# Kernel optimization log

Measured on AMD Instinct MI355X. Metric: run time of the kernel, lower is better.

The kernel has to match this reference:

```python
import jax, jax.numpy as jnp
import numpy as np
import math

SIZE = 2048
N_CLASSES = 16
STEPS = 100
DT = 0.03
GAMMA = 0.125
BETA = 1.0
EIG = 1.0
EPSILON = 0.1


def _make_P(size=SIZE, n_classes=N_CLASSES):
    # Default attractor construction: block indicator columns.
    attr = np.zeros((size, n_classes), dtype=np.float32)
    block = size // n_classes
    for c in range(n_classes):
        attr[c * block:(c + 1) * block, c] = 1.0
    norm_attr = attr / (np.linalg.norm(attr, axis=0, keepdims=True) + 1e-8) ** 2
    return jnp.asarray(norm_attr @ attr.T)  # [size, size] projection onto attractor subspace


def setup_inputs() -> dict:
    key = jax.random.key(0)
    kx, ka, kg, kn = jax.random.split(key, 4)
    x = jax.random.normal(kx, (512, SIZE), dtype=jnp.float32)
    # kaiming_uniform_(a=sqrt(5)) => U(-1/sqrt(fan_in), 1/sqrt(fan_in))
    bound = 1.0 / math.sqrt(SIZE)
    A = jax.random.uniform(ka, (SIZE, SIZE), minval=-bound, maxval=bound, dtype=jnp.float32)
    G = jax.random.uniform(kg, (SIZE, SIZE), minval=-bound, maxval=bound, dtype=jnp.float32)
    noise = jax.random.normal(kn, (STEPS, 512, SIZE), dtype=jnp.float32)
    return {"x": x, "A": A, "G": G, "noise": noise}


def reference(x, A, G, noise):
    P = _make_P()
    antiP = jnp.eye(SIZE, dtype=x.dtype) - P
    B = (A @ antiP + EIG * P).T  # [size, size]
    GT = G.T
    sqrt_dt = math.sqrt(DT)

    def nl(x):
        x2 = x * x
        return x2 / (GAMMA + x2)

    def step(x, n):
        x_dot = -x + BETA * (nl(x) @ B)
        x_new = x + DT * x_dot + sqrt_dt * EPSILON * (n @ GT)
        return x_new, None

    x_final, _ = jax.lax.scan(step, x, noise)
    return x_final
```

## Files before the change

### kernel.cpp

```cpp
#include <hip/hip_runtime.h>
#include <cstdint>


typedef unsigned short ushort_t;
typedef __bf16 bf16x8 __attribute__((ext_vector_type(8)));
typedef float f32x4 __attribute__((ext_vector_type(4)));
typedef unsigned short u16x4 __attribute__((ext_vector_type(4)));
typedef unsigned short u16x8 __attribute__((ext_vector_type(8)));

#define SZ 2048
#define BATCH 512
#define NSTEPS 100

static constexpr float DT = 0.03f;
static constexpr float GAM = 0.125f;
static constexpr float PVAL = (float)(1.0 / (128.0 + 2.2627416997969522e-07));
static constexpr float CNOISE = 0.017320508075688773f;

__device__ __forceinline__ unsigned short f2bf(float f) {
    unsigned int u = __builtin_bit_cast(unsigned int, f);
    return (unsigned short)((u + 0x7fffu + ((u >> 16) & 1u)) >> 16);
}
__device__ __forceinline__ float bf2f(unsigned short h) {
    unsigned int u = ((unsigned int)h) << 16;
    return __builtin_bit_cast(float, u);
}
__device__ __forceinline__ void async16(const void* g, void* l) {
    __builtin_amdgcn_global_load_lds(
        (__attribute__((address_space(1))) void*)(uintptr_t)g,
        (__attribute__((address_space(3))) void*)(uint32_t)(uintptr_t)l,
        16, 0, 0);
}

__global__ __launch_bounds__(256) void conv_kernel(const float* __restrict__ n,
                                                   ushort_t* __restrict__ nb) {
    const size_t i = ((size_t)blockIdx.x * 256 + threadIdx.x) * 4;
    f32x4 v = *(const f32x4*)(n + i);
    u16x4 o;
#pragma unroll
    for (int e = 0; e < 4; ++e) o[e] = f2bf(v[e]);
    *(u16x4*)(nb + i) = o;
}

__global__ __launch_bounds__(256) void prep_kernel(const float* __restrict__ A,
                                                   const float* __restrict__ G,
                                                   ushort_t* __restrict__ BTs,
                                                   ushort_t* __restrict__ Gs) {
    const int n = blockIdx.x;
    const int t = threadIdx.x;
    __shared__ float s16[16];
    const float* arow = A + (size_t)n * SZ;
    f32x4 a0 = *(const f32x4*)(arow + t * 8);
    f32x4 a1 = *(const f32x4*)(arow + t * 8 + 4);
    float ps = a0[0] + a0[1] + a0[2] + a0[3] + a1[0] + a1[1] + a1[2] + a1[3];
#pragma unroll
    for (int m = 1; m < 16; m <<= 1) ps += __shfl_xor(ps, m, 64);
    if ((t & 15) == 0) s16[t >> 4] = ps * PVAL;
    __syncthreads();
    const int seg = t >> 4;
    const float s = s16[seg];
    const float diag = (seg == (n >> 7)) ? PVAL : 0.0f;
    float av[8] = {a0[0], a0[1], a0[2], a0[3], a1[0], a1[1], a1[2], a1[3]};
    u16x8 ov;
#pragma unroll
    for (int i = 0; i < 8; ++i) ov[i] = f2bf(DT * (av[i] - s + diag));
    *(u16x8*)&BTs[(size_t)n * SZ + t * 8] = ov;

    const float* grow = G + (size_t)n * SZ;
    f32x4 g0 = *(const f32x4*)(grow + t * 8);
    f32x4 g1 = *(const f32x4*)(grow + t * 8 + 4);
    float gv[8] = {g0[0], g0[1], g0[2], g0[3], g1[0], g1[1], g1[2], g1[3]};
    u16x8 og;
#pragma unroll
    for (int i = 0; i < 8; ++i) og[i] = f2bf(CNOISE * gv[i]);
    *(u16x8*)&Gs[(size_t)n * SZ + t * 8] = og;
}

__global__ __launch_bounds__(256) void init_kernel(const float* __restrict__ x,
                                                   float* __restrict__ xbuf,
                                                   ushort_t* __restrict__ Y0) {
    const size_t i = ((size_t)blockIdx.x * 256 + threadIdx.x) * 4;
    f32x4 xv = *(const f32x4*)(x + i);
    *(f32x4*)(xbuf + i) = xv;
    u16x4 yv;
#pragma unroll
    for (int e = 0; e < 4; ++e) {
        float x2 = xv[e] * xv[e];
        yv[e] = f2bf(x2 / (GAM + x2));
    }
    *(u16x4*)(Y0 + i) = yv;
}

__global__ __launch_bounds__(256) void zgemm_kernel(const ushort_t* __restrict__ Nb,
                                                    const ushort_t* __restrict__ Gs,
                                                    ushort_t* __restrict__ Z) {
    __shared__ ushort_t sm[16384];
    const int tid = threadIdx.x;
    const int w = tid >> 6, l = tid & 63;
    const int m0 = blockIdx.y << 7, n0 = blockIdx.x << 7;
    const char* Ag = (const char*)Nb + (size_t)m0 * 4096;
    const char* Bg = (const char*)Gs + (size_t)n0 * 4096;
    const int goff = (tid >> 3) * 4096 + (((tid & 7) ^ ((tid >> 3) & 7)) << 4);
    const int loff = tid * 16;
    const int lr = l & 15, q8 = l >> 4;
    const int wm = (w & 1) << 6, wn = (w >> 1) << 6;
    const int swz = lr & 7;
    f32x4 acc[4][4] = {};

    char* sA = (char*)sm;
    char* sB = sA + 16384;
    for (int kk = 0; kk < 32; ++kk) {
        __syncthreads();
        const char* Ac = Ag + kk * 128;
        const char* Bc = Bg + kk * 128;
#pragma unroll
        for (int i = 0; i < 4; ++i) {
            async16(Ac + i * 131072 + goff, sA + i * 4096 + loff);
            async16(Bc + i * 131072 + goff, sB + i * 4096 + loff);
        }
        asm volatile("s_waitcnt vmcnt(0)" ::: "memory");
        __syncthreads();
#pragma unroll
        for (int half = 0; half < 2; ++half) {
            const int qpos = ((((half << 2) | q8) ^ swz) << 4);
            bf16x8 af[4], bfv[4];
#pragma unroll
            for (int f = 0; f < 4; ++f) {
                af[f] = *(const bf16x8*)(sA + (wm + f * 16 + lr) * 128 + qpos);
                bfv[f] = *(const bf16x8*)(sB + (wn + f * 16 + lr) * 128 + qpos);
            }
#pragma unroll
            for (int fr = 0; fr < 4; ++fr)
#pragma unroll
                for (int fc = 0; fc < 4; ++fc)
                    acc[fr][fc] = __builtin_amdgcn_mfma_f32_16x16x32_bf16(
                        af[fr], bfv[fc], acc[fr][fc], 0, 0, 0);
        }
    }
    ushort_t* zr = Z + (size_t)m0 * SZ + n0;
#pragma unroll
    for (int fr = 0; fr < 4; ++fr)
#pragma unroll
        for (int reg = 0; reg < 4; ++reg) {
            const size_t rb = (size_t)(wm + fr * 16 + q8 * 4 + reg) * SZ;
#pragma unroll
            for (int fc = 0; fc < 4; ++fc)
                zr[rb + wn + fc * 16 + lr] = f2bf(acc[fr][fc][reg]);
        }
}

__global__ __launch_bounds__(512, 2) void step_kernel(
    const ushort_t* __restrict__ Ycur, const ushort_t* __restrict__ BTs,
    const ushort_t* __restrict__ Zt, const float* __restrict__ xin,
    float* __restrict__ xout, ushort_t* __restrict__ Ynext) {
    extern __shared__ ushort_t smem[];
    const int tid = threadIdx.x;
    const int w = tid >> 6, l = tid & 63;
    const int m0 = blockIdx.y << 6, n0 = blockIdx.x << 6;

    const char* Ag = (const char*)Ycur + (size_t)m0 * 4096 + w * 512;
    const char* Bg = (const char*)BTs + (size_t)n0 * 4096 + w * 512;
    char* waveLds = (char*)smem + w * 16384;

    const int goffL = (l >> 2) * 4096 + ((((l & 3) ^ ((l >> 3) & 3))) << 4);
    const int loffL = l * 16;
    const int lr = l & 15, q8 = l >> 4;
    const int swz2 = (lr >> 1) & 3;

    f32x4 acc[4][4] = {};

    auto stage = [&](int ci, int b) {
        const char* Ac = Ag + ci * 64;
        const char* Bc = Bg + ci * 64;
        char* dA = waveLds + b * 8192;
        char* dB = dA + 4096;
#pragma unroll
        for (int i = 0; i < 4; ++i) {
            async16(Ac + i * 65536 + goffL, dA + i * 1024 + loffL);
            async16(Bc + i * 65536 + goffL, dB + i * 1024 + loffL);
        }
    };
    auto compute = [&](int b) {
        const char* TA = waveLds + b * 8192;
        const char* TB = TA + 4096;
        const int qpos = ((q8 ^ swz2) << 4);
        bf16x8 af[4], bfv[4];
#pragma unroll
        for (int f = 0; f < 4; ++f) {
            af[f] = *(const bf16x8*)(TA + (f * 16 + lr) * 64 + qpos);
            bfv[f] = *(const bf16x8*)(TB + (f * 16 + lr) * 64 + qpos);
        }
#pragma unroll
        for (int fr = 0; fr < 4; ++fr)
#pragma unroll
            for (int fc = 0; fc < 4; ++fc)
                acc[fr][fc] = __builtin_amdgcn_mfma_f32_16x16x32_bf16(
                    af[fr], bfv[fc], acc[fr][fc], 0, 0, 0);
    };

    stage(0, 0);
#pragma unroll 2
    for (int ci = 0; ci < 8; ++ci) {
        if (ci < 7) {
            stage(ci + 1, (ci + 1) & 1);
            asm volatile("s_waitcnt vmcnt(8)" ::: "memory");
        } else {
            asm volatile("s_waitcnt vmcnt(0)" ::: "memory");
        }
        compute(ci & 1);
    }

    float* redF = (float*)smem;
#pragma unroll
    for (int p = 0; p < 2; ++p) {
        __syncthreads();
#pragma unroll
        for (int fl = 0; fl < 2; ++fl) {
            const int fr = p * 2 + fl;
            const int rl = fl * 16 + q8 * 4;
#pragma unroll
            for (int fc = 0; fc < 4; ++fc) {
                const int c = fc * 16 + lr;
#pragma unroll
                for (int reg = 0; reg < 4; ++reg)
                    redF[w * 2176 + (rl + reg) * 68 + c] = acc[fr][fc][reg];
            }
        }
        __syncthreads();
        {
            const int r = tid >> 4;
            const int c0 = (tid & 15) << 2;
            const int off = r * 68 + c0;
            f32x4 s = *(const f32x4*)&redF[off];
#pragma unroll
            for (int ww = 1; ww < 8; ++ww)
                s = s + *(const f32x4*)&redF[ww * 2176 + off];
            const size_t gb = (size_t)(m0 + p * 32 + r) * SZ + n0 + c0;
            f32x4 xv = *(const f32x4*)(xin + gb);
            u16x4 zb = *(const u16x4*)(Zt + gb);
            f32x4 xn;
#pragma unroll
            for (int e = 0; e < 4; ++e) xn[e] = xv[e] * (1.0f - DT) + s[e] + bf2f(zb[e]);
            *(f32x4*)(xout + gb) = xn;
            u16x4 yv;
#pragma unroll
            for (int e = 0; e < 4; ++e) {
                float x2 = xn[e] * xn[e];
                yv[e] = f2bf(x2 / (GAM + x2));
            }
            *(u16x4*)(Ynext + gb) = yv;
        }
    }
}

extern "C" void kernel_launch(void* const* d_in, const int* in_sizes, int n_in,
                              void* d_out, int out_size, void* d_ws, size_t ws_size,
                              hipStream_t stream) {
    const float* x = (const float*)d_in[0];
    const float* A = (const float*)d_in[1];
    const float* G = (const float*)d_in[2];
    const float* noise = (const float*)d_in[3];
    float* out = (float*)d_out;
    char* ws = (char*)d_ws;

    float* xbuf = (float*)(ws);
    ushort_t* Y0 = (ushort_t*)(ws + ((size_t)4 << 20));
    ushort_t* Y1 = (ushort_t*)(ws + ((size_t)6 << 20));
    ushort_t* BTs = (ushort_t*)(ws + ((size_t)8 << 20));
    ushort_t* Gsc = (ushort_t*)(ws + ((size_t)16 << 20));
    ushort_t* Nb = (ushort_t*)(ws + ((size_t)24 << 20));
    ushort_t* Z = (ushort_t*)(ws + ((size_t)240 << 20));

    (void)hipFuncSetAttribute((const void*)step_kernel,
                              hipFuncAttributeMaxDynamicSharedMemorySize, 131072);

    conv_kernel<<<dim3(102400), dim3(256), 0, stream>>>(noise, Nb);
    prep_kernel<<<dim3(SZ), dim3(256), 0, stream>>>(A, G, BTs, Gsc);
    init_kernel<<<dim3(1024), dim3(256), 0, stream>>>(x, xbuf, Y0);
    zgemm_kernel<<<dim3(16, 400), dim3(256), 0, stream>>>(Nb, Gsc, Z);

    ushort_t* Yc = Y0;
    ushort_t* Yn = Y1;
    for (int t = 0; t < NSTEPS; ++t) {
        float* xo = (t == NSTEPS - 1) ? out : xbuf;
        step_kernel<<<dim3(32, 8), dim3(512), 131072, stream>>>(
            Yc, BTs, Z + (size_t)t * BATCH * SZ, xbuf, xo, Yn);
        ushort_t* tmp = Yc; Yc = Yn; Yn = tmp;
    }
}
```

Baseline: 2.770 ms.

## Fuse noise GEMM into persistent cooperative step kernel with per-row-group barriers

Replaces the separate noise GEMM and the 100 per-step launches with one cooperative persistent kernel. Each block concatenates the K dimension: four waves multiply Y by B and four multiply the noise slice by G, so the noise term is computed inside the step instead of being stored to and reloaded from a large Z buffer. The x state stays in registers across steps, and blocks synchronise only within their 64-row group through atomic counter barriers. This removes launch overhead and the Z and x global traffic, but doubles the K length of every step and adds spin barriers.

```diff
diff --git a/kernel.cpp b/kernel.cpp
--- a/kernel.cpp
+++ b/kernel.cpp
@@ -20,10 +20,6 @@
 __device__ __forceinline__ unsigned short f2bf(float f) {
     unsigned int u = __builtin_bit_cast(unsigned int, f);
     return (unsigned short)((u + 0x7fffu + ((u >> 16) & 1u)) >> 16);
-}
-__device__ __forceinline__ float bf2f(unsigned short h) {
-    unsigned int u = ((unsigned int)h) << 16;
-    return __builtin_bit_cast(float, u);
 }
 __device__ __forceinline__ void async16(const void* g, void* l) {
     __builtin_amdgcn_global_load_lds(
@@ -77,11 +73,10 @@
 }
 
 __global__ __launch_bounds__(256) void init_kernel(const float* __restrict__ x,
-                                                   float* __restrict__ xbuf,
-                                                   ushort_t* __restrict__ Y0) {
+                                                   ushort_t* __restrict__ Y0,
+                                                   unsigned* __restrict__ bar) {
     const size_t i = ((size_t)blockIdx.x * 256 + threadIdx.x) * 4;
     f32x4 xv = *(const f32x4*)(x + i);
-    *(f32x4*)(xbuf + i) = xv;
     u16x4 yv;
 #pragma unroll
     for (int e = 0; e < 4; ++e) {
@@ -89,45 +84,87 @@
         yv[e] = f2bf(x2 / (GAM + x2));
     }
     *(u16x4*)(Y0 + i) = yv;
-}
-
-__global__ __launch_bounds__(256) void zgemm_kernel(const ushort_t* __restrict__ Nb,
-                                                    const ushort_t* __restrict__ Gs,
-                                                    ushort_t* __restrict__ Z) {
-    __shared__ ushort_t sm[16384];
+    if (blockIdx.x == 0) bar[threadIdx.x] = 0u;
+}
+
+__device__ __forceinline__ void group_barrier(unsigned* cnt, unsigned* gen) {
+    __syncthreads();
+    if (threadIdx.x == 0) {
+        __threadfence();
+        unsigned g = atomicAdd(gen, 0u);
+        if (atomicAdd(cnt, 1u) == 31u) {
+            atomicExch(cnt, 0u);
+            __threadfence();
+            atomicAdd(gen, 1u);
+        } else {
+            while (atomicAdd(gen, 0u) == g) __builtin_amdgcn_s_sleep(8);
+        }
+        __threadfence();
+    }
+    __syncthreads();
+}
+
+__global__ __launch_bounds__(512, 2) void persist_kernel(
+    const float* __restrict__ x0,
+    const ushort_t* __restrict__ BTs, const ushort_t* __restrict__ Gs,
+    const ushort_t* __restrict__ Nb,
+    ushort_t* __restrict__ Y0, ushort_t* __restrict__ Y1,
+    float* __restrict__ xout, unsigned* __restrict__ bar) {
+    extern __shared__ ushort_t smem[];
     const int tid = threadIdx.x;
     const int w = tid >> 6, l = tid & 63;
-    const int m0 = blockIdx.y << 7, n0 = blockIdx.x << 7;
-    const char* Ag = (const char*)Nb + (size_t)m0 * 4096;
-    const char* Bg = (const char*)Gs + (size_t)n0 * 4096;
-    const int goff = (tid >> 3) * 4096 + (((tid & 7) ^ ((tid >> 3) & 7)) << 4);
-    const int loff = tid * 16;
+    const int id = blockIdx.x;
+    const int nIdx = (id & 7) | (((id >> 3) & 3) << 3);
+    const int mIdx = id >> 5;
+    const int m0 = mIdx << 6, n0 = nIdx << 6;
+
+    unsigned* cnt = bar + mIdx * 32;
+    unsigned* gen = cnt + 1;
+
+    const char* Bg = (w < 4)
+        ? ((const char*)BTs + (size_t)n0 * 4096 + w * 1024)
+        : ((const char*)Gs + (size_t)n0 * 4096 + (w - 4) * 1024);
+    char* waveLds = (char*)smem + w * 16384;
+
+    const int goffL = (l >> 2) * 4096 + (((l & 3) ^ ((l >> 3) & 3)) << 4);
+    const int loffL = l * 16;
     const int lr = l & 15, q8 = l >> 4;
-    const int wm = (w & 1) << 6, wn = (w >> 1) << 6;
-    const int swz = lr & 7;
-    f32x4 acc[4][4] = {};
-
-    char* sA = (char*)sm;
-    char* sB = sA + 16384;
-    for (int kk = 0; kk < 32; ++kk) {
-        __syncthreads();
-        const char* Ac = Ag + kk * 128;
-        const char* Bc = Bg + kk * 128;
-#pragma unroll
-        for (int i = 0; i < 4; ++i) {
-            async16(Ac + i * 131072 + goff, sA + i * 4096 + loff);
-            async16(Bc + i * 131072 + goff, sB + i * 4096 + loff);
-        }
-        asm volatile("s_waitcnt vmcnt(0)" ::: "memory");
-        __syncthreads();
-#pragma unroll
-        for (int half = 0; half < 2; ++half) {
-            const int qpos = ((((half << 2) | q8) ^ swz) << 4);
+    const int qpos = (q8 ^ ((lr >> 1) & 3)) << 4;
+
+    const int er = tid >> 4;
+    const int ec0 = (tid & 15) << 2;
+    f32x4 xreg[2];
+    xreg[0] = *(const f32x4*)(x0 + (size_t)(m0 + er) * SZ + n0 + ec0);
+    xreg[1] = *(const f32x4*)(x0 + (size_t)(m0 + 32 + er) * SZ + n0 + ec0);
+
+    for (int t = 0; t < NSTEPS; ++t) {
+        const ushort_t* Yc = (t & 1) ? Y1 : Y0;
+        ushort_t* Yn = (t & 1) ? Y0 : Y1;
+        const char* Ag = (w < 4)
+            ? ((const char*)Yc + (size_t)m0 * 4096 + w * 1024)
+            : ((const char*)Nb + (size_t)t * 2097152 + (size_t)m0 * 4096 + (w - 4) * 1024);
+
+        f32x4 acc[4][4] = {};
+
+        auto stage = [&](int ci, int b) {
+            const char* Ac = Ag + ci * 64;
+            const char* Bc = Bg + ci * 64;
+            char* dA = waveLds + b * 8192;
+            char* dB = dA + 4096;
+#pragma unroll
+            for (int i = 0; i < 4; ++i) {
+                async16(Ac + i * 65536 + goffL, dA + i * 1024 + loffL);
+                async16(Bc + i * 65536 + goffL, dB + i * 1024 + loffL);
+            }
+        };
+        auto compute = [&](int b) {
+            const char* TA = waveLds + b * 8192;
+            const char* TB = TA + 4096;
             bf16x8 af[4], bfv[4];
 #pragma unroll
             for (int f = 0; f < 4; ++f) {
-                af[f] = *(const bf16x8*)(sA + (wm + f * 16 + lr) * 128 + qpos);
-                bfv[f] = *(const bf16x8*)(sB + (wn + f * 16 + lr) * 128 + qpos);
+                af[f] = *(const bf16x8*)(TA + (f * 16 + lr) * 64 + qpos);
+                bfv[f] = *(const bf16x8*)(TB + (f * 16 + lr) * 64 + qpos);
             }
 #pragma unroll
             for (int fr = 0; fr < 4; ++fr)
@@ -135,121 +172,61 @@
                 for (int fc = 0; fc < 4; ++fc)
                     acc[fr][fc] = __builtin_amdgcn_mfma_f32_16x16x32_bf16(
                         af[fr], bfv[fc], acc[fr][fc], 0, 0, 0);
+        };
+
+        stage(0, 0);
+#pragma unroll 2
+        for (int ci = 0; ci < 16; ++ci) {
+            if (ci < 15) {
+                stage(ci + 1, (ci + 1) & 1);
+                asm volatile("s_waitcnt vmcnt(8)" ::: "memory");
+            } else {
+                asm volatile("s_waitcnt vmcnt(0)" ::: "memory");
+            }
+            compute(ci & 1);
         }
-    }
-    ushort_t* zr = Z + (size_t)m0 * SZ + n0;
-#pragma unroll
-    for (int fr = 0; fr < 4; ++fr)
-#pragma unroll
-        for (int reg = 0; reg < 4; ++reg) {
-            const size_t rb = (size_t)(wm + fr * 16 + q8 * 4 + reg) * SZ;
-#pragma unroll
-            for (int fc = 0; fc < 4; ++fc)
-                zr[rb + wn + fc * 16 + lr] = f2bf(acc[fr][fc][reg]);
+
+        float* redF = (float*)smem;
+#pragma unroll
+        for (int p = 0; p < 2; ++p) {
+            __syncthreads();
+#pragma unroll
+            for (int fl = 0; fl < 2; ++fl) {
+                const int fr = p * 2 + fl;
+                const int rl = fl * 16 + q8 * 4;
+#pragma unroll
+                for (int fc = 0; fc < 4; ++fc) {
+                    const int c = fc * 16 + lr;
+#pragma unroll
+                    for (int reg = 0; reg < 4; ++reg)
+                        redF[w * 2176 + (rl + reg) * 68 + c] = acc[p * 2 + fl == fr ? fr : fr][fc][reg];
+                }
+            }
+            __syncthreads();
+            {
+                const int off = er * 68 + ec0;
+                f32x4 s = *(const f32x4*)&redF[off];
+#pragma unroll
+                for (int ww = 1; ww < 8; ++ww)
+                    s = s + *(const f32x4*)&redF[ww * 2176 + off];
+                f32x4 xn = xreg[p] * (1.0f - DT) + s;
+                xreg[p] = xn;
+                const size_t gb = (size_t)(m0 + p * 32 + er) * SZ + n0 + ec0;
+                if (t < NSTEPS - 1) {
+                    u16x4 yv;
+#pragma unroll
+                    for (int e = 0; e < 4; ++e) {
+                        float x2 = xn[e] * xn[e];
+                        yv[e] = f2bf(x2 / (GAM + x2));
+                    }
+                    *(u16x4*)(Yn + gb) = yv;
+                } else {
+                    *(f32x4*)(xout + gb) = xn;
+                }
+            }
         }
-}
-
-__global__ __launch_bounds__(512, 2) void step_kernel(
-    const ushort_t* __restrict__ Ycur, const ushort_t* __restrict__ BTs,
-    const ushort_t* __restrict__ Zt, const float* __restrict__ xin,
-    float* __restrict__ xout, ushort_t* __restrict__ Ynext) {
-    extern __shared__ ushort_t smem[];
-    const int tid = threadIdx.x;
-    const int w = tid >> 6, l = tid & 63;
-    const int m0 = blockIdx.y << 6, n0 = blockIdx.x << 6;
-
-    const char* Ag = (const char*)Ycur + (size_t)m0 * 4096 + w * 512;
-    const char* Bg = (const char*)BTs + (size_t)n0 * 4096 + w * 512;
-    char* waveLds = (char*)smem + w * 16384;
-
-    const int goffL = (l >> 2) * 4096 + ((((l & 3) ^ ((l >> 3) & 3))) << 4);
-    const int loffL = l * 16;
-    const int lr = l & 15, q8 = l >> 4;
-    const int swz2 = (lr >> 1) & 3;
-
-    f32x4 acc[4][4] = {};
-
-    auto stage = [&](int ci, int b) {
-        const char* Ac = Ag + ci * 64;
-        const char* Bc = Bg + ci * 64;
-        char* dA = waveLds + b * 8192;
-        char* dB = dA + 4096;
-#pragma unroll
-        for (int i = 0; i < 4; ++i) {
-            async16(Ac + i * 65536 + goffL, dA + i * 1024 + loffL);
-            async16(Bc + i * 65536 + goffL, dB + i * 1024 + loffL);
-        }
-    };
-    auto compute = [&](int b) {
-        const char* TA = waveLds + b * 8192;
-        const char* TB = TA + 4096;
-        const int qpos = ((q8 ^ swz2) << 4);
-        bf16x8 af[4], bfv[4];
-#pragma unroll
-        for (int f = 0; f < 4; ++f) {
-            af[f] = *(const bf16x8*)(TA + (f * 16 + lr) * 64 + qpos);
-            bfv[f] = *(const bf16x8*)(TB + (f * 16 + lr) * 64 + qpos);
-        }
-#pragma unroll
-        for (int fr = 0; fr < 4; ++fr)
-#pragma unroll
-            for (int fc = 0; fc < 4; ++fc)
-                acc[fr][fc] = __builtin_amdgcn_mfma_f32_16x16x32_bf16(
-                    af[fr], bfv[fc], acc[fr][fc], 0, 0, 0);
-    };
-
-    stage(0, 0);
-#pragma unroll 2
-    for (int ci = 0; ci < 8; ++ci) {
-        if (ci < 7) {
-            stage(ci + 1, (ci + 1) & 1);
-            asm volatile("s_waitcnt vmcnt(8)" ::: "memory");
-        } else {
-            asm volatile("s_waitcnt vmcnt(0)" ::: "memory");
-        }
-        compute(ci & 1);
-    }
-
-    float* redF = (float*)smem;
-#pragma unroll
-    for (int p = 0; p < 2; ++p) {
-        __syncthreads();
-#pragma unroll
-        for (int fl = 0; fl < 2; ++fl) {
-            const int fr = p * 2 + fl;
-            const int rl = fl * 16 + q8 * 4;
-#pragma unroll
-            for (int fc = 0; fc < 4; ++fc) {
-                const int c = fc * 16 + lr;
-#pragma unroll
-                for (int reg = 0; reg < 4; ++reg)
-                    redF[w * 2176 + (rl + reg) * 68 + c] = acc[fr][fc][reg];
-            }
-        }
-        __syncthreads();
-        {
-            const int r = tid >> 4;
-            const int c0 = (tid & 15) << 2;
-            const int off = r * 68 + c0;
-            f32x4 s = *(const f32x4*)&redF[off];
-#pragma unroll
-            for (int ww = 1; ww < 8; ++ww)
-                s = s + *(const f32x4*)&redF[ww * 2176 + off];
-            const size_t gb = (size_t)(m0 + p * 32 + r) * SZ + n0 + c0;
-            f32x4 xv = *(const f32x4*)(xin + gb);
-            u16x4 zb = *(const u16x4*)(Zt + gb);
-            f32x4 xn;
-#pragma unroll
-            for (int e = 0; e < 4; ++e) xn[e] = xv[e] * (1.0f - DT) + s[e] + bf2f(zb[e]);
-            *(f32x4*)(xout + gb) = xn;
-            u16x4 yv;
-#pragma unroll
-            for (int e = 0; e < 4; ++e) {
-                float x2 = xn[e] * xn[e];
-                yv[e] = f2bf(x2 / (GAM + x2));
-            }
-            *(u16x4*)(Ynext + gb) = yv;
-        }
+
+        if (t < NSTEPS - 1) group_barrier(cnt, gen);
     }
 }
 
@@ -263,28 +240,22 @@
     float* out = (float*)d_out;
     char* ws = (char*)d_ws;
 
-    float* xbuf = (float*)(ws);
-    ushort_t* Y0 = (ushort_t*)(ws + ((size_t)4 << 20));
-    ushort_t* Y1 = (ushort_t*)(ws + ((size_t)6 << 20));
-    ushort_t* BTs = (ushort_t*)(ws + ((size_t)8 << 20));
-    ushort_t* Gsc = (ushort_t*)(ws + ((size_t)16 << 20));
-    ushort_t* Nb = (ushort_t*)(ws + ((size_t)24 << 20));
-    ushort_t* Z = (ushort_t*)(ws + ((size_t)240 << 20));
-
-    (void)hipFuncSetAttribute((const void*)step_kernel,
+    unsigned* bar = (unsigned*)(ws);
+    ushort_t* Y0 = (ushort_t*)(ws + ((size_t)1 << 20));
+    ushort_t* Y1 = (ushort_t*)(ws + ((size_t)3 << 20));
+    ushort_t* BTs = (ushort_t*)(ws + ((size_t)5 << 20));
+    ushort_t* Gsc = (ushort_t*)(ws + ((size_t)13 << 20));
+    ushort_t* Nb = (ushort_t*)(ws + ((size_t)21 << 20));
+
+    (void)hipFuncSetAttribute((const void*)persist_kernel,
                               hipFuncAttributeMaxDynamicSharedMemorySize, 131072);
 
     conv_kernel<<<dim3(102400), dim3(256), 0, stream>>>(noise, Nb);
     prep_kernel<<<dim3(SZ), dim3(256), 0, stream>>>(A, G, BTs, Gsc);
-    init_kernel<<<dim3(1024), dim3(256), 0, stream>>>(x, xbuf, Y0);
-    zgemm_kernel<<<dim3(16, 400), dim3(256), 0, stream>>>(Nb, Gsc, Z);
-
-    ushort_t* Yc = Y0;
-    ushort_t* Yn = Y1;
-    for (int t = 0; t < NSTEPS; ++t) {
-        float* xo = (t == NSTEPS - 1) ? out : xbuf;
-        step_kernel<<<dim3(32, 8), dim3(512), 131072, stream>>>(
-            Yc, BTs, Z + (size_t)t * BATCH * SZ, xbuf, xo, Yn);
-        ushort_t* tmp = Yc; Yc = Yn; Yn = tmp;
-    }
-}
+    init_kernel<<<dim3(1024), dim3(256), 0, stream>>>(x, Y0, bar);
+
+    void* args[] = {(void*)&x, (void*)&BTs, (void*)&Gsc, (void*)&Nb,
+                    (void*)&Y0, (void*)&Y1, (void*)&out, (void*)&bar};
+    (void)hipLaunchCooperativeKernel((const void*)persist_kernel, dim3(256), dim3(512),
+                                     args, 131072, stream);
+}
```

Result: slower. 3.970 ms (+43.3%).
